# Optimization experiments

Hardware: AMD Instinct MI355X
Metric: run time of the kernel (lower is better)

The kernel has to match this reference:

```python
import jax, jax.numpy as jnp
import numpy as np

ATOM = 8          # atom_size
STRIDE = 4
NB_ATOMS = 256
LMBDA = 0.1       # l1 prox weight (prox_params)
NONDIFF = 20      # nondiff_steps (run under stop_gradient, mirroring torch.no_grad)
DIFF = 5          # diff_steps


def setup_inputs() -> dict:
    key = jax.random.key(0)
    k1, k2 = jax.random.split(key)
    y = jax.random.normal(k1, (8, 3, 256, 256), dtype=jnp.float32)
    # atoms ~ N(0,1)/sqrt(nb_channels*atom_size^2), as in __init__ with init='random'
    atoms = jax.random.normal(k2, (NB_ATOMS, 3, ATOM, ATOM), dtype=jnp.float32) / np.float32(np.sqrt(3 * ATOM * ATOM))
    return {"y": y, "atoms": atoms}


def _forward(y, atoms):
    B, C, H, W = y.shape
    a, s = ATOM, STRIDE
    Hp = (H - a) // s + 1
    Wp = (W - a) // s + 1
    D = C * a * a

    # patch row/col index grids: rows[ph, i] = ph*s + i
    rows = (jnp.arange(Hp) * s)[:, None] + jnp.arange(a)          # [Hp, a]
    cols = (jnp.arange(Wp) * s)[:, None] + jnp.arange(a)          # [Wp, a]
    R4 = rows[:, :, None, None]                                    # [Hp, a, 1, 1]
    C4 = cols[None, None, :, :]                                    # [1, 1, Wp, a]

    # unfold: extract overlapping patches -> [B, C, Hp, a, Wp, a] -> [N, D] (channel-major, matching torch)
    p6 = y[:, :, R4, C4]
    p = p6.transpose(0, 2, 4, 1, 3, 5).reshape(B * Hp * Wp, D)     # N = B*Hp*Wp

    mean = jnp.mean(p, axis=1, keepdims=True)                      # per-patch mean
    p = p - mean

    # l2-normalize atoms
    A = atoms.reshape(NB_ATOMS, D)
    A = A / jnp.linalg.norm(A, axis=1, keepdims=True)              # [nA, D]

    X = A @ A.T                                                    # [nA, nA] Gram matrix
    q = A @ p.T                                                    # [nA, N]
    L = jnp.linalg.norm(X, 2)                                      # spectral norm (Lipschitz const)
    thr = LMBDA / L

    def ista_step(c, _):
        c = c - (X @ c - q) / L
        c = jnp.sign(c) * jnp.maximum(jnp.abs(c) - thr, 0.0)       # soft-threshold prox
        return c, None

    c0 = jnp.zeros((NB_ATOMS, q.shape[1]), dtype=q.dtype)
    c, _ = jax.lax.scan(ista_step, c0, None, length=NONDIFF)
    c = jax.lax.stop_gradient(c)                                    # torch.no_grad() warmup
    c, _ = jax.lax.scan(ista_step, c, None, length=DIFF)

    # reconstruct patches: einsum('ij,il->jl') = c.T @ A, add mean back
    rec = c.T @ A + mean                                            # [N, D]
    p6r = rec.reshape(B, Hp, Wp, C, a, a).transpose(0, 3, 1, 4, 2, 5)  # [B, C, Hp, a, Wp, a]

    # fold: overlap-add patches back to image
    out = jnp.zeros((B, C, H, W), dtype=y.dtype).at[:, :, R4, C4].add(p6r)
    counts = jnp.zeros((H, W), dtype=y.dtype).at[R4, C4].add(
        jnp.ones((Hp, a, Wp, a), dtype=y.dtype))                    # overlap divisors
    return out / counts


def reference(y, atoms):
    return _forward(y, atoms)
```

## Files before the change

kernel.cpp:

```cpp
#include <hip/hip_runtime.h>
#include <math.h>

#define NPATCH 31752
#define TILE   64
#define PSTR   200
#define MSTR   200

typedef _Float16 f16;
typedef __attribute__((ext_vector_type(2))) _Float16 f16x2;
typedef __attribute__((ext_vector_type(4))) _Float16 f16x4;
typedef __attribute__((ext_vector_type(8))) _Float16 f16x8;
typedef __attribute__((ext_vector_type(2))) __fp16   hf16x2;
typedef __attribute__((ext_vector_type(4))) float    f32x4;
#define MFMA16 __builtin_amdgcn_mfma_f32_16x16x32_f16

union HU { f16x2 h; hf16x2 g; unsigned u; };

__device__ __forceinline__ f16x2 pk2(float a, float b)
{
    HU r; r.g = __builtin_amdgcn_cvt_pkrtz(a, b);
    return r.h;
}

__device__ __forceinline__ f16x2 shrink2(f16x2 v, f16x2 thr2)
{
    HU a; a.h = v;
    unsigned sgn = a.u & 0x80008000u;
    a.u &= 0x7FFF7FFFu;
    f16x2 t = a.h - thr2;
    t = __builtin_elementwise_max(t, (f16x2)(f16)0);
    HU r; r.h = t; r.u |= sgn;
    return r.h;
}

__global__ __launch_bounds__(512, 1)
void lchain_kernel(const float* __restrict__ atoms,
                   float* __restrict__ A, float* __restrict__ As,
                   f16* __restrict__ Ap, f16* __restrict__ Ab,
                   float* __restrict__ scal)
{
    __shared__ __align__(16) f16 mls[2 * 192 * MSTR];
    __shared__ float red[8];
    __shared__ float trc[16];
    const int tid = threadIdx.x, wv = tid >> 6, lane = tid & 63;
    const int quad = lane >> 4, l16 = lane & 15;

    {
        float* ldsf = (float*)mls;
        for (int c = 0; c < 2; ++c) {
            const float4* src4 = (const float4*)(atoms + c * 128 * 192);
            float4* dst4 = (float4*)ldsf;
            #pragma unroll
            for (int k = 0; k < 12; ++k)
                dst4[tid + k * 512] = src4[tid + k * 512];
            __syncthreads();
            #pragma unroll 4
            for (int rr = 0; rr < 16; ++rr) {
                int lr = wv * 16 + rr;
                int b  = c * 128 + lr;
                float v0 = ldsf[lr * 192 + lane];
                float v1 = ldsf[lr * 192 +  64 + lane];
                float v2 = ldsf[lr * 192 + 128 + lane];
                float s = v0 * v0 + v1 * v1 + v2 * v2;
                float r = v0 + v1 + v2;
                #pragma unroll
                for (int m = 1; m < 64; m <<= 1) {
                    s += __shfl_xor(s, m, 64);
                    r += __shfl_xor(r, m, 64);
                }
                float rn = 1.0f / sqrtf(s);
                if (lane == 0) As[b] = r * rn;
                const int I = b >> 4, l16b = b & 15;
                const int ksb = b >> 5, qb = (b >> 3) & 3, jb = b & 7;
                float vv[3] = { v0, v1, v2 };
                #pragma unroll
                for (int u = 0; u < 3; ++u) {
                    int t = u * 64 + lane;
                    float a = vv[u] * rn;
                    A[b * 192 + t] = a;
                    f16 ah = (f16)a;
                    int ks = t >> 5, q = (t >> 3) & 3, j = t & 7;
                    Ap[((I * 6 + ks) * 64 + q * 16 + l16b) * 8 + j] = ah;
                    int dt = t >> 4, dl = t & 15;
                    Ab[((dt * 8 + ksb) * 64 + qb * 16 + dl) * 8 + jb] = ah;
                }
            }
            __syncthreads();
        }
    }
    __threadfence_block();

    const int g3 = (wv >> 1) * 3;
    const int h6 = (wv & 1) * 6;
    const f16x8* AbV = (const f16x8*)Ab;

    f32x4 acc[3][6];
    #pragma unroll
    for (int it = 0; it < 3; ++it)
        #pragma unroll
        for (int jj = 0; jj < 6; ++jj) acc[it][jj] = (f32x4){0,0,0,0};
    for (int ks = 0; ks < 8; ++ks) {
        f16x8 bf[6];
        #pragma unroll
        for (int jj = 0; jj < 6; ++jj) bf[jj] = AbV[((h6 + jj)*8 + ks)*64 + lane];
        #pragma unroll
        for (int it = 0; it < 3; ++it) {
            f16x8 af = AbV[((g3 + it)*8 + ks)*64 + lane];
            #pragma unroll
            for (int jj = 0; jj < 6; ++jj)
                acc[it][jj] = MFMA16(af, bf[jj], acc[it][jj], 0, 0, 0);
        }
    }
    #pragma unroll
    for (int it = 0; it < 3; ++it) {
        int I = g3 + it;
        #pragma unroll
        for (int jj = 0; jj < 6; ++jj) {
            int J = h6 + jj;
            f16x2 lo = pk2(acc[it][jj][0], acc[it][jj][1]);
            f16x2 hi = pk2(acc[it][jj][2], acc[it][jj][3]);
            f16x4 cc; cc[0]=lo[0]; cc[1]=lo[1]; cc[2]=hi[0]; cc[3]=hi[1];
            *(f16x4*)&mls[(J*16 + l16)*MSTR + I*16 + quad*4] = cc;
        }
    }
    __syncthreads();

    float rprev = 1.0f;
    for (int t = 1; t <= 8; ++t) {
        const f16* src = mls + ((t & 1) ^ 1) * (192 * MSTR);
        f16*       dst = mls + (t & 1) * (192 * MSTR);
        const float inv = 1.0f / rprev;
        const float inv2 = inv * inv;

        f32x4 a2[3][6];
        #pragma unroll
        for (int it = 0; it < 3; ++it)
            #pragma unroll
            for (int jj = 0; jj < 6; ++jj) a2[it][jj] = (f32x4){0,0,0,0};
        for (int ksd = 0; ksd < 6; ++ksd) {
            f16x8 bf[6];
            #pragma unroll
            for (int jj = 0; jj < 6; ++jj)
                bf[jj] = *(const f16x8*)&src[((h6 + jj)*16 + l16)*MSTR + ksd*32 + quad*8];
            #pragma unroll
            for (int it = 0; it < 3; ++it) {
                f16x8 af = *(const f16x8*)&src[((g3 + it)*16 + l16)*MSTR + ksd*32 + quad*8];
                #pragma unroll
                for (int jj = 0; jj < 6; ++jj)
                    a2[it][jj] = MFMA16(af, bf[jj], a2[it][jj], 0, 0, 0);
            }
        }
        float dsum = 0.0f;
        #pragma unroll
        for (int it = 0; it < 3; ++it) {
            int I = g3 + it;
            #pragma unroll
            for (int jj = 0; jj < 6; ++jj) {
                int J = h6 + jj;
                float v0 = a2[it][jj][0] * inv2;
                float v1 = a2[it][jj][1] * inv2;
                float v2 = a2[it][jj][2] * inv2;
                float v3 = a2[it][jj][3] * inv2;
                f16x2 lo = pk2(v0, v1);
                f16x2 hi = pk2(v2, v3);
                f16x4 cc; cc[0]=lo[0]; cc[1]=lo[1]; cc[2]=hi[0]; cc[3]=hi[1];
                *(f16x4*)&dst[(J*16 + l16)*MSTR + I*16 + quad*4] = cc;
                if (J == I) {
                    int dg = l16 - quad*4;
                    if (dg >= 0 && dg < 4)
                        dsum += (dg == 0 ? v0 : dg == 1 ? v1 : dg == 2 ? v2 : v3);
                }
            }
        }
        #pragma unroll
        for (int m = 1; m < 64; m <<= 1) dsum += __shfl_xor(dsum, m, 64);
        if (lane == 0) red[wv] = dsum;
        __syncthreads();
        float r = red[0] + red[1] + red[2] + red[3]
                + red[4] + red[5] + red[6] + red[7];
        if (tid == 0) trc[t] = r;
        rprev = r;
        __syncthreads();
    }
    if (tid == 0) {
        float a = 0.0f;
        #pragma unroll
        for (int u = 1; u <= 8; ++u) a += exp2f(-(float)u) * log2f(trc[u]);
        float L = exp2f(a);
        scal[16] = 1.0f / L;
        scal[17] = 0.1f / L;
    }
}

__global__ void gpack_kernel(const float* __restrict__ A, const float* __restrict__ scal,
                             f16* __restrict__ Gp, float* __restrict__ out, int out_n)
{
    __shared__ float arow[192];
    __shared__ float xrow[256];
    {
        float4* o4 = (float4*)out;
        int idx = blockIdx.x * blockDim.x + threadIdx.x;
        int tot4 = out_n >> 2;
        for (int u = idx; u < tot4; u += gridDim.x * blockDim.x)
            o4[u] = (float4){0.f, 0.f, 0.f, 0.f};
        for (int u = (tot4 << 2) + idx; u < out_n; u += gridDim.x * blockDim.x)
            out[u] = 0.f;
    }
    int i = blockIdx.x, j = threadIdx.x;
    const float invL = scal[16];
    if (j < 192) arow[j] = A[i*192 + j];
    __syncthreads();
    float s = 0.0f;
    #pragma unroll 4
    for (int d = 0; d < 192; d += 4) {
        float4 av = *(const float4*)&A[j*192 + d];
        s += arow[d]*av.x + arow[d+1]*av.y + arow[d+2]*av.z + arow[d+3]*av.w;
    }
    xrow[j] = (i == j ? 1.0f : 0.0f) - s * invL;
    __syncthreads();
    if (j < 32) {
        int ks = j >> 2, q = j & 3;
        f16x8 h;
        #pragma unroll
        for (int u = 0; u < 8; ++u) h[u] = (f16)xrow[ks*32 + q*8 + u];
        int I = i >> 4, lane = q*16 + (i & 15);
        *(f16x8*)&Gp[(((I*8 + ks)*64) + lane)*8] = h;
    }
}

__global__ __launch_bounds__(512, 4)
void mega_kernel(const float* __restrict__ y,
                 const f16* __restrict__ Gp, const f16* __restrict__ Ap,
                 const f16* __restrict__ Ab, const float* __restrict__ As,
                 const float* __restrict__ scal, float* __restrict__ out)
{
    __shared__ f16      p_lds[TILE * PSTR];
    __shared__ f16      c_lds[2 * 16 * 512];
    __shared__ float    mean_lds[TILE];
    __shared__ unsigned pco[TILE];

    const int tid  = threadIdx.x;
    const int base = blockIdx.x * TILE;
    const int wv = tid >> 6, lane = tid & 63, quad = lane >> 4, l16 = lane & 15;
    const float invL = scal[16];
    const float thr  = scal[17];
    const f16x2 thr2 = { (f16)thr, (f16)thr };

    #define CWADDR(st, rt, ct) \
        ((st)*8192 + ((ct)*8 + wv)*512 \
         + (((rt)*2 + (quad>>1))*16 + l16)*8 + (quad&1)*4)
    #define LDB0(st, ks) (*(const f16x8*)&c_lds[(st)*8192 + (ks)*512 + lane*8])
    #define LDB1(st, ks) (*(const f16x8*)&c_lds[(st)*8192 + (8 + (ks))*512 + lane*8])

    f16x8 greg[2][8];
    {
        const f16x8* GpV = (const f16x8*)Gp;
        #pragma unroll
        for (int rt = 0; rt < 2; ++rt)
            #pragma unroll
            for (int ks = 0; ks < 8; ++ks)
                greg[rt][ks] = GpV[((wv*2 + rt)*8 + ks)*64 + lane];
    }

    {
        int n_l = tid >> 3, qq = tid & 7;
        int n = base + n_l; if (n >= NPATCH) n = NPATCH - 1;
        int b = n / 3969, rem = n - b * 3969;
        int r = rem / 63, sc = rem - r * 63;
        float s = 0.0f;
        #pragma unroll
        for (int u = 0; u < 3; ++u) {
            int d  = qq * 24 + u * 8;
            int ch = d >> 6, id = (d & 63) >> 3;
            const float* src = &y[((b*3 + ch)*256 + (r*4 + id))*256 + sc*4];
            float4 a = *(const float4*)src;
            float4 bq = *(const float4*)(src + 4);
            s += a.x + a.y + a.z + a.w + bq.x + bq.y + bq.z + bq.w;
            f16x8 h = { (f16)a.x, (f16)a.y, (f16)a.z, (f16)a.w,
                        (f16)bq.x, (f16)bq.y, (f16)bq.z, (f16)bq.w };
            *(f16x8*)&p_lds[n_l * PSTR + d] = h;
        }
        s += __shfl_xor(s, 1, 64);
        s += __shfl_xor(s, 2, 64);
        s += __shfl_xor(s, 4, 64);
        if (qq == 0) {
            mean_lds[n_l] = s * (1.0f / 192.0f);
            pco[n_l] = ((unsigned)b << 16) | ((unsigned)r << 8) | (unsigned)sc;
        }
    }
    __syncthreads();

    f16x2 qslo[2][2][2], qshi[2][2][2];
    const f16x8* ApV = (const f16x8*)Ap;
    #pragma unroll
    for (int st = 0; st < 2; ++st) {
        f32x4 qf[2][2];
        #pragma unroll
        for (int rt = 0; rt < 2; ++rt)
            #pragma unroll
            for (int ct = 0; ct < 2; ++ct) qf[rt][ct] = (f32x4){0,0,0,0};
        #pragma unroll
        for (int ks = 0; ks < 6; ++ks) {
            f16x8 bf[2];
            #pragma unroll
            for (int ct = 0; ct < 2; ++ct)
                bf[ct] = *(const f16x8*)&p_lds[(st*32 + ct*16 + l16)*PSTR + ks*32 + quad*8];
            #pragma unroll
            for (int rt = 0; rt < 2; ++rt) {
                f16x8 af = ApV[((wv*2 + rt)*6 + ks)*64 + lane];
                #pragma unroll
                for (int ct = 0; ct < 2; ++ct)
                    qf[rt][ct] = MFMA16(af, bf[ct], qf[rt][ct], 0, 0, 0);
            }
        }
        #pragma unroll
        for (int rt = 0; rt < 2; ++rt) {
            float4 av = *(const float4*)&As[(wv*2 + rt)*16 + quad*4];
            #pragma unroll
            for (int ct = 0; ct < 2; ++ct) {
                float mn = mean_lds[st*32 + ct*16 + l16];
                float q0 = (qf[rt][ct][0] - mn*av.x) * invL;
                float q1 = (qf[rt][ct][1] - mn*av.y) * invL;
                float q2 = (qf[rt][ct][2] - mn*av.z) * invL;
                float q3 = (qf[rt][ct][3] - mn*av.w) * invL;
                f16x2 lo = pk2(q0, q1);
                f16x2 hi = pk2(q2, q3);
                qslo[st][rt][ct] = lo;  qshi[st][rt][ct] = hi;
                f16x2 clo = shrink2(lo, thr2);
                f16x2 chi = shrink2(hi, thr2);
                f16x4 cc; cc[0]=clo[0]; cc[1]=clo[1]; cc[2]=chi[0]; cc[3]=chi[1];
                *(f16x4*)&c_lds[CWADDR(st, rt, ct)] = cc;
            }
        }
    }
    __syncthreads();

    f16x8 pa0 = LDB0(0,0), pa1 = LDB1(0,0), pa2 = LDB0(0,1), pa3 = LDB1(0,1);
    for (int it = 0; it < 24; ++it) {
        f32x4 af[2][2];
        #pragma unroll
        for (int rt = 0; rt < 2; ++rt)
            #pragma unroll
            for (int ct = 0; ct < 2; ++ct) af[rt][ct] = (f32x4){0,0,0,0};
        __builtin_amdgcn_s_setprio(1);
        #pragma unroll
        for (int ks = 0; ks < 8; ++ks) {
            f16x8 b0 = (ks == 0) ? pa0 : (ks == 1) ? pa2 : LDB0(0, ks);
            f16x8 b1 = (ks == 0) ? pa1 : (ks == 1) ? pa3 : LDB1(0, ks);
            #pragma unroll
            for (int rt = 0; rt < 2; ++rt) {
                af[rt][0] = MFMA16(greg[rt][ks], b0, af[rt][0], 0, 0, 0);
                af[rt][1] = MFMA16(greg[rt][ks], b1, af[rt][1], 0, 0, 0);
            }
        }
        __builtin_amdgcn_s_setprio(0);
        __syncthreads();
        f16x8 pb0 = LDB0(1,0), pb1 = LDB1(1,0), pb2 = LDB0(1,1), pb3 = LDB1(1,1);
        #pragma unroll
        for (int rt = 0; rt < 2; ++rt)
            #pragma unroll
            for (int ct = 0; ct < 2; ++ct) {
                f16x2 vlo = pk2(af[rt][ct][0], af[rt][ct][1]) + qslo[0][rt][ct];
                f16x2 vhi = pk2(af[rt][ct][2], af[rt][ct][3]) + qshi[0][rt][ct];
                vlo = shrink2(vlo, thr2);
                vhi = shrink2(vhi, thr2);
                f16x4 cc; cc[0]=vlo[0]; cc[1]=vlo[1]; cc[2]=vhi[0]; cc[3]=vhi[1];
                *(f16x4*)&c_lds[CWADDR(0, rt, ct)] = cc;
            }
        #pragma unroll
        for (int rt = 0; rt < 2; ++rt)
            #pragma unroll
            for (int ct = 0; ct < 2; ++ct) af[rt][ct] = (f32x4){0,0,0,0};
        __builtin_amdgcn_s_setprio(1);
        #pragma unroll
        for (int ks = 0; ks < 8; ++ks) {
            f16x8 b0 = (ks == 0) ? pb0 : (ks == 1) ? pb2 : LDB0(1, ks);
            f16x8 b1 = (ks == 0) ? pb1 : (ks == 1) ? pb3 : LDB1(1, ks);
            #pragma unroll
            for (int rt = 0; rt < 2; ++rt) {
                af[rt][0] = MFMA16(greg[rt][ks], b0, af[rt][0], 0, 0, 0);
                af[rt][1] = MFMA16(greg[rt][ks], b1, af[rt][1], 0, 0, 0);
            }
        }
        __builtin_amdgcn_s_setprio(0);
        __syncthreads();
        pa0 = LDB0(0,0); pa1 = LDB1(0,0); pa2 = LDB0(0,1); pa3 = LDB1(0,1);
        #pragma unroll
        for (int rt = 0; rt < 2; ++rt)
            #pragma unroll
            for (int ct = 0; ct < 2; ++ct) {
                f16x2 vlo = pk2(af[rt][ct][0], af[rt][ct][1]) + qslo[1][rt][ct];
                f16x2 vhi = pk2(af[rt][ct][2], af[rt][ct][3]) + qshi[1][rt][ct];
                vlo = shrink2(vlo, thr2);
                vhi = shrink2(vhi, thr2);
                f16x4 cc; cc[0]=vlo[0]; cc[1]=vlo[1]; cc[2]=vhi[0]; cc[3]=vhi[1];
                *(f16x4*)&c_lds[CWADDR(1, rt, ct)] = cc;
            }
    }
    __syncthreads();

    const int nt = wv >> 2, dtb = 3 * (wv & 3);
    const f16x8* AbV = (const f16x8*)Ab;
    #pragma unroll
    for (int st = 0; st < 2; ++st) {
        f32x4 rf[3];
        #pragma unroll
        for (int u = 0; u < 3; ++u) rf[u] = (f32x4){0,0,0,0};
        #pragma unroll
        for (int ks = 0; ks < 8; ++ks) {
            f16x8 afr = *(const f16x8*)&c_lds[st*8192 + (nt*8 + ks)*512 + lane*8];
            #pragma unroll
            for (int u = 0; u < 3; ++u) {
                f16x8 bb = AbV[((dtb + u)*8 + ks)*64 + lane];
                rf[u] = MFMA16(afr, bb, rf[u], 0, 0, 0);
            }
        }
        #pragma unroll
        for (int g = 0; g < 4; ++g) {
            int nl = nt*16 + quad*4 + g;
            int n  = base + st*32 + nl;
            if (n < NPATCH) {
                unsigned pc = pco[st*32 + nl];
                int b = pc >> 16, r = (pc >> 8) & 255, sc = pc & 255;
                float mn = mean_lds[st*32 + nl];
                #pragma unroll
                for (int u = 0; u < 3; ++u) {
                    int d  = (dtb + u)*16 + l16;
                    int ch = d >> 6, dh = (d & 63) >> 3, dw = d & 7;
                    int h  = r*4 + dh, w2 = sc*4 + dw;
                    int cnth = min(62, h >> 2)  - (max(h - 4, 0) >> 2) + 1;
                    int cntw = min(62, w2 >> 2) - (max(w2 - 4, 0) >> 2) + 1;
                    float rcp = 1.0f / (float)(cnth * cntw);
                    atomicAdd(&out[((b*3 + ch)*256 + (r*4 + dh))*256 + sc*4 + dw],
                              (rf[u][g] + mn) * rcp);
                }
            }
        }
    }
    #undef CWADDR
    #undef LDB0
    #undef LDB1
}

extern "C" void kernel_launch(void* const* d_in, const int* in_sizes, int n_in,
                              void* d_out, int out_size, void* d_ws, size_t ws_size,
                              hipStream_t stream)
{
    const float* y     = (const float*)d_in[0];
    const float* atoms = (const float*)d_in[1];
    float* out = (float*)d_out;
    float* ws  = (float*)d_ws;

    float* A    = ws;
    float* As   = ws + 49152;
    float* scal = ws + 49408;
    f16*   Ap   = (f16*)(ws + 49440);
    f16*   Ab   = (f16*)(ws + 74016);
    f16*   Gp   = (f16*)(ws + 98592);

    lchain_kernel<<<1, 512, 0, stream>>>(atoms, A, As, Ap, Ab, scal);
    gpack_kernel <<<256, 256, 0, stream>>>(A, scal, Gp, out, out_size);
    mega_kernel  <<<(NPATCH + TILE - 1) / TILE, 512, 0, stream>>>
        (y, Gp, Ap, Ab, As, scal, out);
}
```

Baseline: 215.3 us.

## Fuse setup, Gram, spectral-norm and ISTA stages into one cooperative kernel

Replaces the three-launch pipeline (single-block Lipschitz chain, Gram pack, main ISTA kernel) with one cooperative kernel of 512 blocks using grid.sync. Atom normalisation is spread across 256 blocks, the Gram tiles are built by 16 blocks in parallel with the single-block power chain, and patch loading overlaps that serial chain before the grid barrier. This aims to remove launch gaps and the serialized single-block prologue, at the cost of two grid-wide barriers and a launch that needs all 512 blocks resident at once. The old path stays as a fallback if the cooperative launch fails.

```diff
diff --git a/kernel.cpp b/kernel.cpp
--- a/kernel.cpp
+++ b/kernel.cpp
@@ -1,5 +1,8 @@
 #include <hip/hip_runtime.h>
+#include <hip/hip_cooperative_groups.h>
 #include <math.h>
+
+namespace cg = cooperative_groups;
 
 #define NPATCH 31752
 #define TILE   64
@@ -31,6 +34,405 @@
     t = __builtin_elementwise_max(t, (f16x2)(f16)0);
     HU r; r.h = t; r.u |= sgn;
     return r.h;
+}
+
+__global__ __launch_bounds__(512, 4)
+void fused_kernel(const float* __restrict__ atoms, const float* __restrict__ y,
+                  float* __restrict__ As, f16* __restrict__ Ap,
+                  f16* __restrict__ Ab, f16* __restrict__ Xp,
+                  float* __restrict__ scal, float* __restrict__ out, int out_n)
+{
+    __shared__ __align__(16) unsigned char smem[76800];
+    __shared__ float red[8];
+    __shared__ float trc[16];
+    __shared__ float part[16];
+
+    f16*      p_lds    = (f16*)smem;
+    f16*      c_lds    = (f16*)(smem + 25600);
+    float*    mean_lds = (float*)(smem + 58368);
+    unsigned* pco      = (unsigned*)(smem + 58624);
+    f16*      mM       = (f16*)smem;
+
+    const int tid = threadIdx.x, bid = blockIdx.x;
+    const int wv = tid >> 6, lane = tid & 63, quad = lane >> 4, l16 = lane & 15;
+    const int base = bid * TILE;
+    cg::grid_group grid = cg::this_grid();
+
+    {
+        float4* o4 = (float4*)out;
+        int tot4 = out_n >> 2;
+        for (int u = bid * 512 + tid; u < tot4; u += 512 * 512)
+            o4[u] = (float4){0.f, 0.f, 0.f, 0.f};
+    }
+    float nv = 0.0f;
+    if (bid < 256) {
+        if (tid < 192) nv = atoms[bid * 192 + tid];
+        float s = nv * nv, r = nv;
+        #pragma unroll
+        for (int m = 1; m < 64; m <<= 1) {
+            s += __shfl_xor(s, m, 64);
+            r += __shfl_xor(r, m, 64);
+        }
+        if (lane == 0) { part[wv] = s; part[8 + wv] = r; }
+    }
+    __syncthreads();
+    if (bid < 256 && tid < 192) {
+        float s = part[0] + part[1] + part[2];
+        float r = part[8] + part[9] + part[10];
+        float rn = 1.0f / sqrtf(s);
+        float a  = nv * rn;
+        if (tid == 0) As[bid] = r * rn;
+        f16 ah = (f16)a;
+        {
+            int I = bid >> 4, l16b = bid & 15;
+            int ks = tid >> 5, q = (tid >> 3) & 3, j = tid & 7;
+            Ap[((I*6 + ks)*64 + q*16 + l16b)*8 + j] = ah;
+        }
+        {
+            int dt = tid >> 4, dl = tid & 15;
+            int ks = bid >> 5, q = (bid >> 3) & 3, j = bid & 7;
+            Ab[((dt*8 + ks)*64 + q*16 + dl)*8 + j] = ah;
+        }
+    }
+    __threadfence();
+    grid.sync();
+
+    if (bid == 0) {
+        const int g3 = (wv >> 1) * 3;
+        const int h6 = (wv & 1) * 6;
+        const f16x8* AbV = (const f16x8*)Ab;
+        f32x4 acc[3][6];
+        #pragma unroll
+        for (int it = 0; it < 3; ++it)
+            #pragma unroll
+            for (int jj = 0; jj < 6; ++jj) acc[it][jj] = (f32x4){0,0,0,0};
+        for (int ks = 0; ks < 8; ++ks) {
+            f16x8 bf[6];
+            #pragma unroll
+            for (int jj = 0; jj < 6; ++jj) bf[jj] = AbV[((h6 + jj)*8 + ks)*64 + lane];
+            #pragma unroll
+            for (int it = 0; it < 3; ++it) {
+                f16x8 af = AbV[((g3 + it)*8 + ks)*64 + lane];
+                #pragma unroll
+                for (int jj = 0; jj < 6; ++jj)
+                    acc[it][jj] = MFMA16(af, bf[jj], acc[it][jj], 0, 0, 0);
+            }
+        }
+        #pragma unroll
+        for (int it = 0; it < 3; ++it) {
+            int I = g3 + it;
+            #pragma unroll
+            for (int jj = 0; jj < 6; ++jj) {
+                int J = h6 + jj;
+                f16x2 lo = pk2(acc[it][jj][0], acc[it][jj][1]);
+                f16x2 hi = pk2(acc[it][jj][2], acc[it][jj][3]);
+                f16x4 cc; cc[0]=lo[0]; cc[1]=lo[1]; cc[2]=hi[0]; cc[3]=hi[1];
+                *(f16x4*)&mM[(J*16 + l16)*MSTR + I*16 + quad*4] = cc;
+            }
+        }
+        __syncthreads();
+
+        float rprev = 1.0f;
+        for (int t = 1; t <= 8; ++t) {
+            const float inv = 1.0f / rprev;
+            const float inv2 = inv * inv;
+            f32x4 a2[3][6];
+            #pragma unroll
+            for (int it = 0; it < 3; ++it)
+                #pragma unroll
+                for (int jj = 0; jj < 6; ++jj) a2[it][jj] = (f32x4){0,0,0,0};
+            for (int ksd = 0; ksd < 6; ++ksd) {
+                f16x8 bf[6];
+                #pragma unroll
+                for (int jj = 0; jj < 6; ++jj)
+                    bf[jj] = *(const f16x8*)&mM[((h6 + jj)*16 + l16)*MSTR + ksd*32 + quad*8];
+                #pragma unroll
+                for (int it = 0; it < 3; ++it) {
+                    f16x8 af = *(const f16x8*)&mM[((g3 + it)*16 + l16)*MSTR + ksd*32 + quad*8];
+                    #pragma unroll
+                    for (int jj = 0; jj < 6; ++jj)
+                        a2[it][jj] = MFMA16(af, bf[jj], a2[it][jj], 0, 0, 0);
+                }
+            }
+            __syncthreads();
+            float dsum = 0.0f;
+            #pragma unroll
+            for (int it = 0; it < 3; ++it) {
+                int I = g3 + it;
+                #pragma unroll
+                for (int jj = 0; jj < 6; ++jj) {
+                    int J = h6 + jj;
+                    float v0 = a2[it][jj][0] * inv2;
+                    float v1 = a2[it][jj][1] * inv2;
+                    float v2 = a2[it][jj][2] * inv2;
+                    float v3 = a2[it][jj][3] * inv2;
+                    f16x2 lo = pk2(v0, v1);
+                    f16x2 hi = pk2(v2, v3);
+                    f16x4 cc; cc[0]=lo[0]; cc[1]=lo[1]; cc[2]=hi[0]; cc[3]=hi[1];
+                    *(f16x4*)&mM[(J*16 + l16)*MSTR + I*16 + quad*4] = cc;
+                    if (J == I) {
+                        int dg = l16 - quad*4;
+                        if (dg >= 0 && dg < 4)
+                            dsum += (dg == 0 ? v0 : dg == 1 ? v1 : dg == 2 ? v2 : v3);
+                    }
+                }
+            }
+            #pragma unroll
+            for (int m = 1; m < 64; m <<= 1) dsum += __shfl_xor(dsum, m, 64);
+            if (lane == 0) red[wv] = dsum;
+            __syncthreads();
+            float r = red[0] + red[1] + red[2] + red[3]
+                    + red[4] + red[5] + red[6] + red[7];
+            if (tid == 0) trc[t] = r;
+            rprev = r;
+            __syncthreads();
+        }
+        if (tid == 0) {
+            float a = 0.0f;
+            #pragma unroll
+            for (int u = 1; u <= 8; ++u) a += exp2f(-(float)u) * log2f(trc[u]);
+            float L = exp2f(a);
+            scal[16] = 1.0f / L;
+            scal[17] = 0.1f / L;
+        }
+        __syncthreads();
+    } else if (bid <= 16) {
+        const int I = bid - 1;
+        const f16x8* ApV = (const f16x8*)Ap;
+        #pragma unroll
+        for (int jj = 0; jj < 2; ++jj) {
+            int J = wv*2 + jj;
+            f32x4 acc = (f32x4){0,0,0,0};
+            #pragma unroll
+            for (int ks = 0; ks < 6; ++ks) {
+                f16x8 af = ApV[(I*6 + ks)*64 + lane];
+                f16x8 bf = ApV[(J*6 + ks)*64 + lane];
+                acc = MFMA16(af, bf, acc, 0, 0, 0);
+            }
+            f16x2 lo = pk2(acc[0], acc[1]);
+            f16x2 hi = pk2(acc[2], acc[3]);
+            f16x4 cc; cc[0]=lo[0]; cc[1]=lo[1]; cc[2]=hi[0]; cc[3]=hi[1];
+            int ks2 = I >> 1;
+            int q2  = (2*I + (quad >> 1)) & 3;
+            int j2  = (quad & 1) * 4;
+            *(f16x4*)&Xp[(((J*8 + ks2)*64) + q2*16 + l16)*8 + j2] = cc;
+        }
+    }
+    {
+        int n_l = tid >> 3, qq = tid & 7;
+        int n = base + n_l; if (n >= NPATCH) n = NPATCH - 1;
+        int b = n / 3969, rem = n - b * 3969;
+        int r = rem / 63, sc = rem - r * 63;
+        float s = 0.0f;
+        #pragma unroll
+        for (int u = 0; u < 3; ++u) {
+            int d  = qq * 24 + u * 8;
+            int ch = d >> 6, id = (d & 63) >> 3;
+            const float* src = &y[((b*3 + ch)*256 + (r*4 + id))*256 + sc*4];
+            float4 a = *(const float4*)src;
+            float4 bq = *(const float4*)(src + 4);
+            s += a.x + a.y + a.z + a.w + bq.x + bq.y + bq.z + bq.w;
+            f16x8 h = { (f16)a.x, (f16)a.y, (f16)a.z, (f16)a.w,
+                        (f16)bq.x, (f16)bq.y, (f16)bq.z, (f16)bq.w };
+            *(f16x8*)&p_lds[n_l * PSTR + d] = h;
+        }
+        s += __shfl_xor(s, 1, 64);
+        s += __shfl_xor(s, 2, 64);
+        s += __shfl_xor(s, 4, 64);
+        if (qq == 0) {
+            mean_lds[n_l] = s * (1.0f / 192.0f);
+            pco[n_l] = ((unsigned)b << 16) | ((unsigned)r << 8) | (unsigned)sc;
+        }
+    }
+    __threadfence();
+    grid.sync();
+
+    const float invL = scal[16];
+    const float thr  = scal[17];
+    const f16x2 thr2 = { (f16)thr, (f16)thr };
+
+    #define CWADDR(st, rt, ct) \
+        ((st)*8192 + ((ct)*8 + wv)*512 \
+         + (((rt)*2 + (quad>>1))*16 + l16)*8 + (quad&1)*4)
+    #define LDB0(st, ks) (*(const f16x8*)&c_lds[(st)*8192 + (ks)*512 + lane*8])
+    #define LDB1(st, ks) (*(const f16x8*)&c_lds[(st)*8192 + (8 + (ks))*512 + lane*8])
+
+    f16x8 greg[2][8];
+    {
+        const f16x8* XpV = (const f16x8*)Xp;
+        #pragma unroll
+        for (int rt = 0; rt < 2; ++rt) {
+            int r = (wv*2 + rt)*16 + l16;
+            #pragma unroll
+            for (int ks = 0; ks < 8; ++ks) {
+                f16x8 xv = XpV[((wv*2 + rt)*8 + ks)*64 + lane];
+                float f[8];
+                #pragma unroll
+                for (int j = 0; j < 8; ++j) {
+                    int c = ks*32 + quad*8 + j;
+                    float d = (r == c) ? 1.0f : 0.0f;
+                    f[j] = fmaf(-invL, (float)xv[j], d);
+                }
+                f16x2 p0 = pk2(f[0], f[1]), p1 = pk2(f[2], f[3]);
+                f16x2 p2 = pk2(f[4], f[5]), p3 = pk2(f[6], f[7]);
+                f16x8 gg;
+                gg[0]=p0[0]; gg[1]=p0[1]; gg[2]=p1[0]; gg[3]=p1[1];
+                gg[4]=p2[0]; gg[5]=p2[1]; gg[6]=p3[0]; gg[7]=p3[1];
+                greg[rt][ks] = gg;
+            }
+        }
+    }
+
+    f16x2 qslo[2][2][2], qshi[2][2][2];
+    const f16x8* ApV = (const f16x8*)Ap;
+    #pragma unroll
+    for (int st = 0; st < 2; ++st) {
+        f32x4 qf[2][2];
+        #pragma unroll
+        for (int rt = 0; rt < 2; ++rt)
+            #pragma unroll
+            for (int ct = 0; ct < 2; ++ct) qf[rt][ct] = (f32x4){0,0,0,0};
+        #pragma unroll
+        for (int ks = 0; ks < 6; ++ks) {
+            f16x8 bf[2];
+            #pragma unroll
+            for (int ct = 0; ct < 2; ++ct)
+                bf[ct] = *(const f16x8*)&p_lds[(st*32 + ct*16 + l16)*PSTR + ks*32 + quad*8];
+            #pragma unroll
+            for (int rt = 0; rt < 2; ++rt) {
+                f16x8 af = ApV[((wv*2 + rt)*6 + ks)*64 + lane];
+                #pragma unroll
+                for (int ct = 0; ct < 2; ++ct)
+                    qf[rt][ct] = MFMA16(af, bf[ct], qf[rt][ct], 0, 0, 0);
+            }
+        }
+        #pragma unroll
+        for (int rt = 0; rt < 2; ++rt) {
+            float4 av = *(const float4*)&As[(wv*2 + rt)*16 + quad*4];
+            #pragma unroll
+            for (int ct = 0; ct < 2; ++ct) {
+                float mn = mean_lds[st*32 + ct*16 + l16];
+                float q0 = (qf[rt][ct][0] - mn*av.x) * invL;
+                float q1 = (qf[rt][ct][1] - mn*av.y) * invL;
+                float q2 = (qf[rt][ct][2] - mn*av.z) * invL;
+                float q3 = (qf[rt][ct][3] - mn*av.w) * invL;
+                f16x2 lo = pk2(q0, q1);
+                f16x2 hi = pk2(q2, q3);
+                qslo[st][rt][ct] = lo;  qshi[st][rt][ct] = hi;
+                f16x2 clo = shrink2(lo, thr2);
+                f16x2 chi = shrink2(hi, thr2);
+                f16x4 cc; cc[0]=clo[0]; cc[1]=clo[1]; cc[2]=chi[0]; cc[3]=chi[1];
+                *(f16x4*)&c_lds[CWADDR(st, rt, ct)] = cc;
+            }
+        }
+    }
+    __syncthreads();
+
+    f16x8 pa0 = LDB0(0,0), pa1 = LDB1(0,0), pa2 = LDB0(0,1), pa3 = LDB1(0,1);
+    for (int it = 0; it < 24; ++it) {
+        f32x4 af[2][2];
+        #pragma unroll
+        for (int rt = 0; rt < 2; ++rt)
+            #pragma unroll
+            for (int ct = 0; ct < 2; ++ct) af[rt][ct] = (f32x4){0,0,0,0};
+        __builtin_amdgcn_s_setprio(1);
+        #pragma unroll
+        for (int ks = 0; ks < 8; ++ks) {
+            f16x8 b0 = (ks == 0) ? pa0 : (ks == 1) ? pa2 : LDB0(0, ks);
+            f16x8 b1 = (ks == 0) ? pa1 : (ks == 1) ? pa3 : LDB1(0, ks);
+            #pragma unroll
+            for (int rt = 0; rt < 2; ++rt) {
+                af[rt][0] = MFMA16(greg[rt][ks], b0, af[rt][0], 0, 0, 0);
+                af[rt][1] = MFMA16(greg[rt][ks], b1, af[rt][1], 0, 0, 0);
+            }
+        }
+        __builtin_amdgcn_s_setprio(0);
+        __syncthreads();
+        f16x8 pb0 = LDB0(1,0), pb1 = LDB1(1,0), pb2 = LDB0(1,1), pb3 = LDB1(1,1);
+        #pragma unroll
+        for (int rt = 0; rt < 2; ++rt)
+            #pragma unroll
+            for (int ct = 0; ct < 2; ++ct) {
+                f16x2 vlo = pk2(af[rt][ct][0], af[rt][ct][1]) + qslo[0][rt][ct];
+                f16x2 vhi = pk2(af[rt][ct][2], af[rt][ct][3]) + qshi[0][rt][ct];
+                vlo = shrink2(vlo, thr2);
+                vhi = shrink2(vhi, thr2);
+                f16x4 cc; cc[0]=vlo[0]; cc[1]=vlo[1]; cc[2]=vhi[0]; cc[3]=vhi[1];
+                *(f16x4*)&c_lds[CWADDR(0, rt, ct)] = cc;
+            }
+        #pragma unroll
+        for (int rt = 0; rt < 2; ++rt)
+            #pragma unroll
+            for (int ct = 0; ct < 2; ++ct) af[rt][ct] = (f32x4){0,0,0,0};
+        __builtin_amdgcn_s_setprio(1);
+        #pragma unroll
+        for (int ks = 0; ks < 8; ++ks) {
+            f16x8 b0 = (ks == 0) ? pb0 : (ks == 1) ? pb2 : LDB0(1, ks);
+            f16x8 b1 = (ks == 0) ? pb1 : (ks == 1) ? pb3 : LDB1(1, ks);
+            #pragma unroll
+            for (int rt = 0; rt < 2; ++rt) {
+                af[rt][0] = MFMA16(greg[rt][ks], b0, af[rt][0], 0, 0, 0);
+                af[rt][1] = MFMA16(greg[rt][ks], b1, af[rt][1], 0, 0, 0);
+            }
+        }
+        __builtin_amdgcn_s_setprio(0);
+        __syncthreads();
+        pa0 = LDB0(0,0); pa1 = LDB1(0,0); pa2 = LDB0(0,1); pa3 = LDB1(0,1);
+        #pragma unroll
+        for (int rt = 0; rt < 2; ++rt)
+            #pragma unroll
+            for (int ct = 0; ct < 2; ++ct) {
+                f16x2 vlo = pk2(af[rt][ct][0], af[rt][ct][1]) + qslo[1][rt][ct];
+                f16x2 vhi = pk2(af[rt][ct][2], af[rt][ct][3]) + qshi[1][rt][ct];
+                vlo = shrink2(vlo, thr2);
+                vhi = shrink2(vhi, thr2);
+                f16x4 cc; cc[0]=vlo[0]; cc[1]=vlo[1]; cc[2]=vhi[0]; cc[3]=vhi[1];
+                *(f16x4*)&c_lds[CWADDR(1, rt, ct)] = cc;
+            }
+    }
+    __syncthreads();
+
+    const int nt = wv >> 2, dtb = 3 * (wv & 3);
+    const f16x8* AbV = (const f16x8*)Ab;
+    #pragma unroll
+    for (int st = 0; st < 2; ++st) {
+        f32x4 rf[3];
+        #pragma unroll
+        for (int u = 0; u < 3; ++u) rf[u] = (f32x4){0,0,0,0};
+        #pragma unroll
+        for (int ks = 0; ks < 8; ++ks) {
+            f16x8 afr = *(const f16x8*)&c_lds[st*8192 + (nt*8 + ks)*512 + lane*8];
+            #pragma unroll
+            for (int u = 0; u < 3; ++u) {
+                f16x8 bb = AbV[((dtb + u)*8 + ks)*64 + lane];
+                rf[u] = MFMA16(afr, bb, rf[u], 0, 0, 0);
+            }
+        }
+        #pragma unroll
+        for (int g = 0; g < 4; ++g) {
+            int nl = nt*16 + quad*4 + g;
+            int n  = base + st*32 + nl;
+            if (n < NPATCH) {
+                unsigned pc = pco[st*32 + nl];
+                int b = pc >> 16, r = (pc >> 8) & 255, sc = pc & 255;
+                float mn = mean_lds[st*32 + nl];
+                #pragma unroll
+                for (int u = 0; u < 3; ++u) {
+                    int d  = (dtb + u)*16 + l16;
+                    int ch = d >> 6, dh = (d & 63) >> 3, dw = d & 7;
+                    int h  = r*4 + dh, w2 = sc*4 + dw;
+                    int cnth = min(62, h >> 2)  - (max(h - 4, 0) >> 2) + 1;
+                    int cntw = min(62, w2 >> 2) - (max(w2 - 4, 0) >> 2) + 1;
+                    float rcp = 1.0f / (float)(cnth * cntw);
+                    atomicAdd(&out[((b*3 + ch)*256 + (r*4 + dh))*256 + sc*4 + dw],
+                              (rf[u][g] + mn) * rcp);
+                }
+            }
+        }
+    }
+    #undef CWADDR
+    #undef LDB0
+    #undef LDB1
 }
 
 __global__ __launch_bounds__(512, 1)
@@ -44,7 +446,6 @@
     __shared__ float trc[16];
     const int tid = threadIdx.x, wv = tid >> 6, lane = tid & 63;
     const int quad = lane >> 4, l16 = lane & 15;
-
     {
         float* ldsf = (float*)mls;
         for (int c = 0; c < 2; ++c) {
@@ -89,11 +490,9 @@
         }
     }
     __threadfence_block();
-
     const int g3 = (wv >> 1) * 3;
     const int h6 = (wv & 1) * 6;
     const f16x8* AbV = (const f16x8*)Ab;
-
     f32x4 acc[3][6];
     #pragma unroll
     for (int it = 0; it < 3; ++it)
@@ -124,14 +523,12 @@
         }
     }
     __syncthreads();
-
     float rprev = 1.0f;
     for (int t = 1; t <= 8; ++t) {
         const f16* src = mls + ((t & 1) ^ 1) * (192 * MSTR);
         f16*       dst = mls + (t & 1) * (192 * MSTR);
         const float inv = 1.0f / rprev;
         const float inv2 = inv * inv;
-
         f32x4 a2[3][6];
         #pragma unroll
         for (int it = 0; it < 3; ++it)
@@ -203,8 +600,6 @@
         int tot4 = out_n >> 2;
         for (int u = idx; u < tot4; u += gridDim.x * blockDim.x)
             o4[u] = (float4){0.f, 0.f, 0.f, 0.f};
-        for (int u = (tot4 << 2) + idx; u < out_n; u += gridDim.x * blockDim.x)
-            out[u] = 0.f;
     }
     int i = blockIdx.x, j = threadIdx.x;
     const float invL = scal[16];
@@ -261,7 +656,6 @@
             for (int ks = 0; ks < 8; ++ks)
                 greg[rt][ks] = GpV[((wv*2 + rt)*8 + ks)*64 + lane];
     }
-
     {
         int n_l = tid >> 3, qq = tid & 7;
         int n = base + n_l; if (n >= NPATCH) n = NPATCH - 1;
@@ -456,10 +850,19 @@
     float* scal = ws + 49408;
     f16*   Ap   = (f16*)(ws + 49440);
     f16*   Ab   = (f16*)(ws + 74016);
-    f16*   Gp   = (f16*)(ws + 98592);
-
-    lchain_kernel<<<1, 512, 0, stream>>>(atoms, A, As, Ap, Ab, scal);
-    gpack_kernel <<<256, 256, 0, stream>>>(A, scal, Gp, out, out_size);
-    mega_kernel  <<<(NPATCH + TILE - 1) / TILE, 512, 0, stream>>>
-        (y, Gp, Ap, Ab, As, scal, out);
+    f16*   Xp   = (f16*)(ws + 98592);
+    int    outn = out_size;
+
+    void* kargs[] = { (void*)&atoms, (void*)&y, (void*)&As, (void*)&Ap,
+                      (void*)&Ab, (void*)&Xp, (void*)&scal, (void*)&out,
+                      (void*)&outn };
+    hipError_t e = hipLaunchCooperativeKernel((const void*)fused_kernel,
+                                              dim3(512), dim3(512),
+                                              kargs, 0, stream);
+    if (e != hipSuccess) {
+        lchain_kernel<<<1, 512, 0, stream>>>(atoms, A, As, Ap, Ab, scal);
+        gpack_kernel <<<256, 256, 0, stream>>>(A, scal, Xp, out, outn);
+        mega_kernel  <<<(NPATCH + TILE - 1) / TILE, 512, 0, stream>>>
+            (y, Xp, Ap, Ab, As, scal, out);
+    }
 }
```

Result: slower. 485.0 us (+125.3%).

## Parallelize atom normalization and Gram packing, fold identity-minus-scaling into mega kernel

Applied to the files above, without the earlier changes.

Atom normalization and packing move out of the single-block lchain kernel into a 256-block kernel that also zeroes the output. Extra blocks of lchain compute the Gram matrix with MFMA in f16 and store it packed, which replaces the fp32 gpack kernel. The mega kernel then forms I - X/L from the packed Gram matrix when it loads the operator into registers. This shortens the serial setup chain, at the cost of extra f16 rounding of the Gram entries and some per-block conversion work in the mega kernel.

```diff
diff --git a/kernel.cpp b/kernel.cpp
--- a/kernel.cpp
+++ b/kernel.cpp
@@ -33,62 +33,79 @@
     return r.h;
 }
 
+__global__ void fusedpack_kernel(const float* __restrict__ atoms,
+                                 float* __restrict__ As,
+                                 f16* __restrict__ Ap, f16* __restrict__ Ab,
+                                 float* __restrict__ out, int out_n)
+{
+    __shared__ float part[6];
+    const int b = blockIdx.x, t = threadIdx.x;
+    {
+        float4* o4 = (float4*)out;
+        int tot4 = out_n >> 2;
+        for (int u = b * 192 + t; u < tot4; u += 256 * 192)
+            o4[u] = (float4){0.f, 0.f, 0.f, 0.f};
+    }
+    float v = atoms[b*192 + t];
+    float s = v*v, r = v;
+    #pragma unroll
+    for (int m = 1; m < 64; m <<= 1) { s += __shfl_xor(s, m, 64); r += __shfl_xor(r, m, 64); }
+    const int wv = t >> 6, lane = t & 63;
+    if (lane == 0) { part[wv] = s; part[3 + wv] = r; }
+    __syncthreads();
+    s = part[0] + part[1] + part[2];
+    r = part[3] + part[4] + part[5];
+    float rn = 1.0f / sqrtf(s);
+    float a  = v * rn;
+    if (t == 0) As[b] = r * rn;
+    f16 ah = (f16)a;
+    {
+        int I = b >> 4, l16 = b & 15;
+        int ks = t >> 5, q = (t >> 3) & 3, j = t & 7;
+        Ap[(((I*6 + ks)*64) + q*16 + l16)*8 + j] = ah;
+    }
+    {
+        int dt = t >> 4, dl = t & 15;
+        int ks = b >> 5, q = (b >> 3) & 3, j = b & 7;
+        Ab[(((dt*8 + ks)*64) + q*16 + dl)*8 + j] = ah;
+    }
+    (void)lane;
+}
+
 __global__ __launch_bounds__(512, 1)
-void lchain_kernel(const float* __restrict__ atoms,
-                   float* __restrict__ A, float* __restrict__ As,
-                   f16* __restrict__ Ap, f16* __restrict__ Ab,
-                   float* __restrict__ scal)
+void lchain_kernel(const f16* __restrict__ Ab, const f16* __restrict__ Ap,
+                   f16* __restrict__ Xp, float* __restrict__ scal)
 {
     __shared__ __align__(16) f16 mls[2 * 192 * MSTR];
     __shared__ float red[8];
     __shared__ float trc[16];
-    const int tid = threadIdx.x, wv = tid >> 6, lane = tid & 63;
+    const int tid = threadIdx.x, bid = blockIdx.x;
+    const int wv = tid >> 6, lane = tid & 63;
     const int quad = lane >> 4, l16 = lane & 15;
 
-    {
-        float* ldsf = (float*)mls;
-        for (int c = 0; c < 2; ++c) {
-            const float4* src4 = (const float4*)(atoms + c * 128 * 192);
-            float4* dst4 = (float4*)ldsf;
-            #pragma unroll
-            for (int k = 0; k < 12; ++k)
-                dst4[tid + k * 512] = src4[tid + k * 512];
-            __syncthreads();
-            #pragma unroll 4
-            for (int rr = 0; rr < 16; ++rr) {
-                int lr = wv * 16 + rr;
-                int b  = c * 128 + lr;
-                float v0 = ldsf[lr * 192 + lane];
-                float v1 = ldsf[lr * 192 +  64 + lane];
-                float v2 = ldsf[lr * 192 + 128 + lane];
-                float s = v0 * v0 + v1 * v1 + v2 * v2;
-                float r = v0 + v1 + v2;
-                #pragma unroll
-                for (int m = 1; m < 64; m <<= 1) {
-                    s += __shfl_xor(s, m, 64);
-                    r += __shfl_xor(r, m, 64);
-                }
-                float rn = 1.0f / sqrtf(s);
-                if (lane == 0) As[b] = r * rn;
-                const int I = b >> 4, l16b = b & 15;
-                const int ksb = b >> 5, qb = (b >> 3) & 3, jb = b & 7;
-                float vv[3] = { v0, v1, v2 };
-                #pragma unroll
-                for (int u = 0; u < 3; ++u) {
-                    int t = u * 64 + lane;
-                    float a = vv[u] * rn;
-                    A[b * 192 + t] = a;
-                    f16 ah = (f16)a;
-                    int ks = t >> 5, q = (t >> 3) & 3, j = t & 7;
-                    Ap[((I * 6 + ks) * 64 + q * 16 + l16b) * 8 + j] = ah;
-                    int dt = t >> 4, dl = t & 15;
-                    Ab[((dt * 8 + ksb) * 64 + qb * 16 + dl) * 8 + jb] = ah;
-                }
-            }
-            __syncthreads();
-        }
-    }
-    __threadfence_block();
+    if (bid > 0) {
+        const int I = bid - 1;
+        const f16x8* ApV = (const f16x8*)Ap;
+        #pragma unroll
+        for (int jj = 0; jj < 2; ++jj) {
+            int J = wv*2 + jj;
+            f32x4 acc = (f32x4){0,0,0,0};
+            #pragma unroll
+            for (int ks = 0; ks < 6; ++ks) {
+                f16x8 af = ApV[(I*6 + ks)*64 + lane];
+                f16x8 bf = ApV[(J*6 + ks)*64 + lane];
+                acc = MFMA16(af, bf, acc, 0, 0, 0);
+            }
+            f16x2 lo = pk2(acc[0], acc[1]);
+            f16x2 hi = pk2(acc[2], acc[3]);
+            f16x4 cc; cc[0]=lo[0]; cc[1]=lo[1]; cc[2]=hi[0]; cc[3]=hi[1];
+            int ks2 = I >> 1;
+            int q2  = (2*I + (quad >> 1)) & 3;
+            int j2  = (quad & 1) * 4;
+            *(f16x4*)&Xp[(((J*8 + ks2)*64) + q2*16 + l16)*8 + j2] = cc;
+        }
+        return;
+    }
 
     const int g3 = (wv >> 1) * 3;
     const int h6 = (wv & 1) * 6;
@@ -192,45 +209,9 @@
     }
 }
 
-__global__ void gpack_kernel(const float* __restrict__ A, const float* __restrict__ scal,
-                             f16* __restrict__ Gp, float* __restrict__ out, int out_n)
-{
-    __shared__ float arow[192];
-    __shared__ float xrow[256];
-    {
-        float4* o4 = (float4*)out;
-        int idx = blockIdx.x * blockDim.x + threadIdx.x;
-        int tot4 = out_n >> 2;
-        for (int u = idx; u < tot4; u += gridDim.x * blockDim.x)
-            o4[u] = (float4){0.f, 0.f, 0.f, 0.f};
-        for (int u = (tot4 << 2) + idx; u < out_n; u += gridDim.x * blockDim.x)
-            out[u] = 0.f;
-    }
-    int i = blockIdx.x, j = threadIdx.x;
-    const float invL = scal[16];
-    if (j < 192) arow[j] = A[i*192 + j];
-    __syncthreads();
-    float s = 0.0f;
-    #pragma unroll 4
-    for (int d = 0; d < 192; d += 4) {
-        float4 av = *(const float4*)&A[j*192 + d];
-        s += arow[d]*av.x + arow[d+1]*av.y + arow[d+2]*av.z + arow[d+3]*av.w;
-    }
-    xrow[j] = (i == j ? 1.0f : 0.0f) - s * invL;
-    __syncthreads();
-    if (j < 32) {
-        int ks = j >> 2, q = j & 3;
-        f16x8 h;
-        #pragma unroll
-        for (int u = 0; u < 8; ++u) h[u] = (f16)xrow[ks*32 + q*8 + u];
-        int I = i >> 4, lane = q*16 + (i & 15);
-        *(f16x8*)&Gp[(((I*8 + ks)*64) + lane)*8] = h;
-    }
-}
-
 __global__ __launch_bounds__(512, 4)
 void mega_kernel(const float* __restrict__ y,
-                 const f16* __restrict__ Gp, const f16* __restrict__ Ap,
+                 const f16* __restrict__ Xp, const f16* __restrict__ Ap,
                  const f16* __restrict__ Ab, const float* __restrict__ As,
                  const float* __restrict__ scal, float* __restrict__ out)
 {
@@ -254,12 +235,28 @@
 
     f16x8 greg[2][8];
     {
-        const f16x8* GpV = (const f16x8*)Gp;
-        #pragma unroll
-        for (int rt = 0; rt < 2; ++rt)
-            #pragma unroll
-            for (int ks = 0; ks < 8; ++ks)
-                greg[rt][ks] = GpV[((wv*2 + rt)*8 + ks)*64 + lane];
+        const f16x8* XpV = (const f16x8*)Xp;
+        #pragma unroll
+        for (int rt = 0; rt < 2; ++rt) {
+            int r = (wv*2 + rt)*16 + l16;
+            #pragma unroll
+            for (int ks = 0; ks < 8; ++ks) {
+                f16x8 xv = XpV[((wv*2 + rt)*8 + ks)*64 + lane];
+                float f[8];
+                #pragma unroll
+                for (int j = 0; j < 8; ++j) {
+                    int c = ks*32 + quad*8 + j;
+                    float d = (r == c) ? 1.0f : 0.0f;
+                    f[j] = fmaf(-invL, (float)xv[j], d);
+                }
+                f16x2 p0 = pk2(f[0], f[1]), p1 = pk2(f[2], f[3]);
+                f16x2 p2 = pk2(f[4], f[5]), p3 = pk2(f[6], f[7]);
+                f16x8 gg;
+                gg[0]=p0[0]; gg[1]=p0[1]; gg[2]=p1[0]; gg[3]=p1[1];
+                gg[4]=p2[0]; gg[5]=p2[1]; gg[6]=p3[0]; gg[7]=p3[1];
+                greg[rt][ks] = gg;
+            }
+        }
     }
 
     {
@@ -451,15 +448,15 @@
     float* out = (float*)d_out;
     float* ws  = (float*)d_ws;
 
-    float* A    = ws;
     float* As   = ws + 49152;
     float* scal = ws + 49408;
     f16*   Ap   = (f16*)(ws + 49440);
     f16*   Ab   = (f16*)(ws + 74016);
-    f16*   Gp   = (f16*)(ws + 98592);
-
-    lchain_kernel<<<1, 512, 0, stream>>>(atoms, A, As, Ap, Ab, scal);
-    gpack_kernel <<<256, 256, 0, stream>>>(A, scal, Gp, out, out_size);
-    mega_kernel  <<<(NPATCH + TILE - 1) / TILE, 512, 0, stream>>>
-        (y, Gp, Ap, Ab, As, scal, out);
-}
+    f16*   Xp   = (f16*)(ws + 98592);
+    int    outn = out_size;
+
+    fusedpack_kernel<<<256, 192, 0, stream>>>(atoms, As, Ap, Ab, out, outn);
+    lchain_kernel   <<<17, 512,  0, stream>>>(Ab, Ap, Xp, scal);
+    mega_kernel     <<<(NPATCH + TILE - 1) / TILE, 512, 0, stream>>>
+        (y, Xp, Ap, Ab, As, scal, out);
+}
```

Result: faster. 195.1 us (-9.4%).
